# Kernel optimization log

Measured on AMD Instinct MI355X. Metric: run time of the kernel, lower is better.

The kernel has to match this reference:

```python
import math
import jax, jax.numpy as jnp
import numpy as np

FS = 96000.0
N_BIQUADS = 16
HPF_FREQ_RANGE = (20.0, 500.0)
LPF_FREQ_RANGE = (5000.0, 20000.0)
SHELF_FREQ_RANGE = (50.0, 16000.0)
PEAK_FREQ_RANGE = (100.0, 15000.0)
Q_RANGE = (0.5, 16.0)
GAIN_RANGE = (-24.0, 24.0)
BROADBAND_RANGE = (-60.0, 0.0)


def _denorm_log(norm, lo, hi):
    return jnp.exp(math.log(lo) + norm * (math.log(hi) - math.log(lo)))


def _coef_highpass(fc, Q):
    w0 = 2.0 * math.pi * fc / FS
    alpha = jnp.sin(w0) / (2.0 * Q)
    c = jnp.cos(w0)
    b0 = (1 + c) / 2; b1 = -(1 + c); b2 = (1 + c) / 2
    a0 = 1 + alpha; a1 = -2 * c; a2 = 1 - alpha
    return b0 / a0, b1 / a0, b2 / a0, a1 / a0, a2 / a0


def _coef_lowpass(fc, Q):
    w0 = 2.0 * math.pi * fc / FS
    alpha = jnp.sin(w0) / (2.0 * Q)
    c = jnp.cos(w0)
    b0 = (1 - c) / 2; b1 = 1 - c; b2 = (1 - c) / 2
    a0 = 1 + alpha; a1 = -2 * c; a2 = 1 - alpha
    return b0 / a0, b1 / a0, b2 / a0, a1 / a0, a2 / a0


def _coef_lowshelf(fc, gain_db, Q):
    A = 10.0 ** (gain_db / 40.0)
    w0 = 2.0 * math.pi * fc / FS
    alpha = jnp.sin(w0) / (2.0 * Q)
    c = jnp.cos(w0)
    sA = jnp.sqrt(A)
    b0 = A * (A + 1 - (A - 1) * c + 2 * sA * alpha)
    b1 = 2 * A * (A - 1 - (A + 1) * c)
    b2 = A * (A + 1 - (A - 1) * c - 2 * sA * alpha)
    a0 = A + 1 + (A - 1) * c + 2 * sA * alpha
    a1 = -2 * (A - 1 + (A + 1) * c)
    a2 = A + 1 + (A - 1) * c - 2 * sA * alpha
    return b0 / a0, b1 / a0, b2 / a0, a1 / a0, a2 / a0


def _coef_highshelf(fc, gain_db, Q):
    A = 10.0 ** (gain_db / 40.0)
    w0 = 2.0 * math.pi * fc / FS
    alpha = jnp.sin(w0) / (2.0 * Q)
    c = jnp.cos(w0)
    sA = jnp.sqrt(A)
    b0 = A * (A + 1 + (A - 1) * c + 2 * sA * alpha)
    b1 = -2 * A * (A - 1 + (A + 1) * c)
    b2 = A * (A + 1 + (A - 1) * c - 2 * sA * alpha)
    a0 = A + 1 - (A - 1) * c + 2 * sA * alpha
    a1 = 2 * (A - 1 - (A + 1) * c)
    a2 = A + 1 - (A - 1) * c - 2 * sA * alpha
    return b0 / a0, b1 / a0, b2 / a0, a1 / a0, a2 / a0


def _coef_peak(fc, gain_db, Q):
    A = 10.0 ** (gain_db / 40.0)
    w0 = 2.0 * math.pi * fc / FS
    alpha = jnp.sin(w0) / (2.0 * Q)
    c = jnp.cos(w0)
    b0 = 1 + alpha * A; b1 = -2 * c; b2 = 1 - alpha * A
    a0 = 1 + alpha / A; a1 = -2 * c; a2 = 1 - alpha / A
    return b0 / a0, b1 / a0, b2 / a0, a1 / a0, a2 / a0


def _biquad(x, coefs):
    # x: (B, T); coefs: 5 arrays of shape (B,)
    b0, b1, b2, a1, a2 = coefs

    def step(carry, xt):  # xt: (B,)
        s1, s2 = carry
        y = b0 * xt + s1
        return (b1 * xt - a1 * y + s2, b2 * xt - a2 * y), y

    z = jnp.zeros(x.shape[0], x.dtype)
    _, ys = jax.lax.scan(step, (z, z), x.T)  # ys: (T, B)
    return ys.T


def _chain(audio, params):
    B = audio.shape[0]
    bp = params[:, :N_BIQUADS * 3].reshape(B, N_BIQUADS, 3)
    bb_lo, bb_hi = BROADBAND_RANGE
    in_db = bb_lo + params[:, -2] * (bb_hi - bb_lo)
    out_db = bb_lo + params[:, -1] * (bb_hi - bb_lo)
    x = audio * (10.0 ** (in_db / 20.0))[:, None]

    for i in range(N_BIQUADS):
        fn, gn, qn = bp[:, i, 0], bp[:, i, 1], bp[:, i, 2]
        Q = _denorm_log(qn, *Q_RANGE)
        gain = GAIN_RANGE[0] + gn * (GAIN_RANGE[1] - GAIN_RANGE[0])
        if i == 0:  # HPF
            coefs = _coef_highpass(_denorm_log(fn, *HPF_FREQ_RANGE), Q)
        elif i == 15:  # LPF
            coefs = _coef_lowpass(_denorm_log(fn, *LPF_FREQ_RANGE), Q)
        elif i == 1:  # low shelf
            coefs = _coef_lowshelf(_denorm_log(fn, *SHELF_FREQ_RANGE), gain, Q)
        elif i == 14:  # high shelf
            coefs = _coef_highshelf(_denorm_log(fn, *SHELF_FREQ_RANGE), gain, Q)
        else:  # peaking EQ
            coefs = _coef_peak(_denorm_log(fn, *PEAK_FREQ_RANGE), gain, Q)
        x = _biquad(x, coefs)

    return x * (10.0 ** (out_db / 20.0))[:, None]


def setup_inputs() -> dict:
    key = jax.random.key(0)
    k1, k2 = jax.random.split(key)
    audio = jax.random.normal(k1, (16, 262144), dtype=jnp.float32)
    params = jax.random.uniform(k2, (16, 50), dtype=jnp.float32)
    return {"audio": audio, "params": params}


def reference(audio, params):
    return _chain(audio, params)
```

## Files before the change

### kernel.cpp

```cpp
#include <hip/hip_runtime.h>
#include <math.h>

#define BATCH   16
#define T_LEN   262144
#define NB      16
#define L       64
#define GRP     64
#define SUB     8
#define NSUB    512
#define NSUP    32
#define NG      64
#define NCHUNK  4096
#define XSTRIDE 68

#define DPI 3.14159265358979323846264338327950288

#define OFF_COEF  0
#define OFF_A64   1536
#define OFF_A512  17920
#define OFF_A8K   34304
#define OFF_QEND  50688
#define OFF_SARR  312832
#define OFF_P     574976

__device__ inline void stage_coefs(int i, double fn, double gn, double qn,
                                   double& B0, double& B1, double& B2,
                                   double& A1, double& A2) {
    const double FS = 96000.0;
    double Q    = exp(log(0.5) + qn * (log(16.0) - log(0.5)));
    double gain = -24.0 + gn * 48.0;
    double lo, hi;
    if (i == 0)            { lo = 20.0;   hi = 500.0;   }
    else if (i == 15)      { lo = 5000.0; hi = 20000.0; }
    else if (i == 1 || i == 14) { lo = 50.0; hi = 16000.0; }
    else                   { lo = 100.0;  hi = 15000.0; }
    double fc    = exp(log(lo) + fn * (log(hi) - log(lo)));
    double w0    = 2.0 * DPI * fc / FS;
    double alpha = sin(w0) / (2.0 * Q);
    double c     = cos(w0);
    double b0, b1, b2, a0, a1, a2;
    if (i == 0) {
        b0 = (1.0 + c) * 0.5; b1 = -(1.0 + c); b2 = (1.0 + c) * 0.5;
        a0 = 1.0 + alpha; a1 = -2.0 * c; a2 = 1.0 - alpha;
    } else if (i == 15) {
        b0 = (1.0 - c) * 0.5; b1 = 1.0 - c; b2 = (1.0 - c) * 0.5;
        a0 = 1.0 + alpha; a1 = -2.0 * c; a2 = 1.0 - alpha;
    } else if (i == 1) {
        double A = pow(10.0, gain / 40.0), sA = sqrt(A);
        b0 = A * ((A + 1.0) - (A - 1.0) * c + 2.0 * sA * alpha);
        b1 = 2.0 * A * ((A - 1.0) - (A + 1.0) * c);
        b2 = A * ((A + 1.0) - (A - 1.0) * c - 2.0 * sA * alpha);
        a0 = (A + 1.0) + (A - 1.0) * c + 2.0 * sA * alpha;
        a1 = -2.0 * ((A - 1.0) + (A + 1.0) * c);
        a2 = (A + 1.0) + (A - 1.0) * c - 2.0 * sA * alpha;
    } else if (i == 14) {
        double A = pow(10.0, gain / 40.0), sA = sqrt(A);
        b0 = A * ((A + 1.0) + (A - 1.0) * c + 2.0 * sA * alpha);
        b1 = -2.0 * A * ((A - 1.0) + (A + 1.0) * c);
        b2 = A * ((A + 1.0) + (A - 1.0) * c - 2.0 * sA * alpha);
        a0 = (A + 1.0) - (A - 1.0) * c + 2.0 * sA * alpha;
        a1 = 2.0 * ((A - 1.0) - (A + 1.0) * c);
        a2 = (A + 1.0) - (A - 1.0) * c - 2.0 * sA * alpha;
    } else {
        double A = pow(10.0, gain / 40.0);
        b0 = 1.0 + alpha * A; b1 = -2.0 * c; b2 = 1.0 - alpha * A;
        a0 = 1.0 + alpha / A; a1 = -2.0 * c; a2 = 1.0 - alpha / A;
    }
    B0 = b0 / a0; B1 = b1 / a0; B2 = b2 / a0; A1 = a1 / a0; A2 = a2 / a0;
}

__global__ __launch_bounds__(512) void k0_setup(const float* __restrict__ params,
                                                float* __restrict__ coefs,
                                                float* __restrict__ A64,
                                                float* __restrict__ A512,
                                                float* __restrict__ A8K) {
    int b = blockIdx.x;
    int t = threadIdx.x;
    __shared__ double cf[NB][5];
    __shared__ double M1[32 * 32];
    __shared__ double M2[32 * 32];

    if (t < NB) {
        double B0, B1, B2, A1, A2;
        stage_coefs(t, (double)params[b * 50 + t * 3 + 0],
                       (double)params[b * 50 + t * 3 + 1],
                       (double)params[b * 50 + t * 3 + 2], B0, B1, B2, A1, A2);
        float f0 = (float)B0, f1 = (float)B1, f2 = (float)B2, f3 = (float)A1, f4 = (float)A2;
        cf[t][0] = (double)f0; cf[t][1] = (double)f1; cf[t][2] = (double)f2;
        cf[t][3] = (double)f3; cf[t][4] = (double)f4;
        float* cp = coefs + b * 96 + t * 5;
        cp[0] = f0; cp[1] = f1; cp[2] = f2; cp[3] = f3; cp[4] = f4;
    }
    if (t == NB) {
        double indb = -60.0 + (double)params[b * 50 + 48] * 60.0;
        coefs[b * 96 + 80] = (float)pow(10.0, indb / 20.0);
    }
    if (t == NB + 1) {
        double outdb = -60.0 + (double)params[b * 50 + 49] * 60.0;
        coefs[b * 96 + 81] = (float)pow(10.0, outdb / 20.0);
    }
    __syncthreads();

    if (t < 32) {
        double s1[NB], s2[NB];
#pragma unroll
        for (int i = 0; i < NB; i++) {
            s1[i] = (t == 2 * i) ? 1.0 : 0.0;
            s2[i] = (t == 2 * i + 1) ? 1.0 : 0.0;
        }
        double u = 0.0;
#pragma unroll
        for (int i = 0; i < NB; i++) {
            double y  = cf[i][0] * u + s1[i];
            double n1 = cf[i][1] * u - cf[i][3] * y + s2[i];
            double n2 = cf[i][2] * u - cf[i][4] * y;
            s1[i] = n1; s2[i] = n2; u = y;
        }
#pragma unroll
        for (int i = 0; i < NB; i++) {
            M1[(2 * i) * 32 + t]     = s1[i];
            M1[(2 * i + 1) * 32 + t] = s2[i];
        }
    }
    __syncthreads();

    int c  = t & 31;
    int r0 = t >> 5;
    double* src = M1;
    double* dst = M2;
    for (int sq = 0; sq < 13; sq++) {
        double acc0 = 0.0, acc1 = 0.0;
        for (int k = 0; k < 32; k++) {
            double bv = src[k * 32 + c];
            acc0 += src[r0 * 32 + k] * bv;
            acc1 += src[(r0 + 16) * 32 + k] * bv;
        }
        dst[r0 * 32 + c]        = acc0;
        dst[(r0 + 16) * 32 + c] = acc1;
        __syncthreads();
        { double* tmp = src; src = dst; dst = tmp; }
        float* out_m = (sq == 5) ? A64 : (sq == 8) ? A512 : (sq == 12) ? A8K : nullptr;
        if (out_m) {
            int i0 = r0 * 32 + c, i1 = (r0 + 16) * 32 + c;
            out_m[b * 1024 + i0] = (float)src[i0];
            out_m[b * 1024 + i1] = (float)src[i1];
        }
        __syncthreads();
    }
}

__device__ __forceinline__ void bc_step4(float* qldsw, int row, int cb,
                                         const float* ar,
                                         float p0, float p1, float p2, float p3,
                                         float& q0, float& q1, float& q2, float& q3) {
    qldsw[(cb + 0) * 32 + row] = q0;
    qldsw[(cb + 1) * 32 + row] = q1;
    qldsw[(cb + 2) * 32 + row] = q2;
    qldsw[(cb + 3) * 32 + row] = q3;
    const float* qb = qldsw + cb * 32;
    float a0 = p0, b0 = 0.f, a1 = p1, b1 = 0.f;
    float a2 = p2, b2 = 0.f, a3 = p3, b3 = 0.f;
#pragma unroll
    for (int t4 = 0; t4 < 8; t4++) {
        float4 v0 = *(const float4*)(qb + 0 * 32 + 4 * t4);
        float4 v1 = *(const float4*)(qb + 1 * 32 + 4 * t4);
        float4 v2 = *(const float4*)(qb + 2 * 32 + 4 * t4);
        float4 v3 = *(const float4*)(qb + 3 * 32 + 4 * t4);
        a0 = fmaf(ar[4 * t4 + 0], v0.x, a0); b0 = fmaf(ar[4 * t4 + 1], v0.y, b0);
        a0 = fmaf(ar[4 * t4 + 2], v0.z, a0); b0 = fmaf(ar[4 * t4 + 3], v0.w, b0);
        a1 = fmaf(ar[4 * t4 + 0], v1.x, a1); b1 = fmaf(ar[4 * t4 + 1], v1.y, b1);
        a1 = fmaf(ar[4 * t4 + 2], v1.z, a1); b1 = fmaf(ar[4 * t4 + 3], v1.w, b1);
        a2 = fmaf(ar[4 * t4 + 0], v2.x, a2); b2 = fmaf(ar[4 * t4 + 1], v2.y, b2);
        a2 = fmaf(ar[4 * t4 + 2], v2.z, a2); b2 = fmaf(ar[4 * t4 + 3], v2.w, b2);
        a3 = fmaf(ar[4 * t4 + 0], v3.x, a3); b3 = fmaf(ar[4 * t4 + 1], v3.y, b3);
        a3 = fmaf(ar[4 * t4 + 2], v3.z, a3); b3 = fmaf(ar[4 * t4 + 3], v3.w, b3);
    }
    q0 = a0 + b0; q1 = a1 + b1; q2 = a2 + b2; q3 = a3 + b3;
}

__device__ __forceinline__ float mv_step_rl(const float* ar, float q, float addv) {
    int qi = __float_as_int(q);
    float qb[32];
#pragma unroll
    for (int t = 0; t < 32; t++)
        qb[t] = __int_as_float(__builtin_amdgcn_readlane(qi, t));
    float acc0 = addv, acc1 = 0.f;
#pragma unroll
    for (int t = 0; t < 32; t += 2) {
        acc0 = fmaf(ar[t], qb[t], acc0);
        acc1 = fmaf(ar[t + 1], qb[t + 1], acc1);
    }
    return acc0 + acc1;
}

__device__ __forceinline__ void load_row32(const float* base, int row, float* ar) {
    const float4* a4 = (const float4*)(base + row * 32);
#pragma unroll
    for (int j = 0; j < 8; j++) {
        float4 v = a4[j];
        ar[4 * j + 0] = v.x; ar[4 * j + 1] = v.y;
        ar[4 * j + 2] = v.z; ar[4 * j + 3] = v.w;
    }
}

__device__ __forceinline__ void stage_audio(const float* __restrict__ gbase,
                                            float* __restrict__ xlds, int lane) {
    const float4* g4 = (const float4*)gbase;
    float4 v[16];
#pragma unroll
    for (int it = 0; it < 16; it++) v[it] = g4[it * 64 + lane];
#pragma unroll
    for (int it = 0; it < 16; it++) {
        int idx = it * 64 + lane;
        int ch = idx >> 4, q = idx & 15;
        *(float4*)&xlds[ch * XSTRIDE + q * 4] = v[it];
    }
}

__global__ __launch_bounds__(64, 1) void k1_pass1(const float* __restrict__ audio,
                                                  const float* __restrict__ coefs,
                                                  const float* __restrict__ A64,
                                                  float* __restrict__ P,
                                                  float* __restrict__ Qend) {
    int blk   = blockIdx.x;
    int batch = blk >> 6;
    int grp   = blk & 63;
    int lane  = threadIdx.x;
    int row   = lane & 31;
    int half  = lane >> 5;

    __shared__ float xlds[GRP * XSTRIDE];
    __shared__ float plds[GRP][33];
    __shared__ float qlds[8 * 32];

    stage_audio(audio + (size_t)batch * T_LEN + (size_t)grp * GRP * L, xlds, lane);
    __syncthreads();

    const float* cf = coefs + batch * 96;
    float c0[NB], c1[NB], c2[NB], c3[NB], c4[NB];
#pragma unroll
    for (int i = 0; i < NB; i++) {
        c0[i] = cf[i * 5 + 0]; c1[i] = cf[i * 5 + 1]; c2[i] = cf[i * 5 + 2];
        c3[i] = cf[i * 5 + 3]; c4[i] = cf[i * 5 + 4];
    }
    float ing = cf[80];

    float s1[NB], s2[NB];
#pragma unroll
    for (int i = 0; i < NB; i++) { s1[i] = 0.f; s2[i] = 0.f; }

    float* xrow = &xlds[lane * XSTRIDE];
#pragma unroll 1
    for (int tt = 0; tt < 16; tt++) {
        float4 xv = *(const float4*)&xrow[tt * 4];
        float xs[4] = {xv.x, xv.y, xv.z, xv.w};
#pragma unroll
        for (int j = 0; j < 4; j++) {
            float u = ing * xs[j];
#pragma unroll
            for (int i = 0; i < NB; i++) {
                float y  = fmaf(c0[i], u, s1[i]);
                float n1 = fmaf(c1[i], u, s2[i]); n1 = fmaf(-c3[i], y, n1);
                float n2 = c2[i] * u;             n2 = fmaf(-c4[i], y, n2);
                s1[i] = n1; s2[i] = n2; u = y;
            }
        }
    }

    {
        float* pb = P + ((size_t)(batch * NG + grp)) * 2048;
#pragma unroll
        for (int i = 0; i < NB; i++) {
            pb[(2 * i) * 64 + lane]     = s1[i];
            pb[(2 * i + 1) * 64 + lane] = s2[i];
        }
    }

#pragma unroll
    for (int i = 0; i < NB; i++) {
        plds[lane][2 * i]     = s1[i];
        plds[lane][2 * i + 1] = s2[i];
    }
    __syncthreads();

    float ar[32];
    load_row32(A64 + batch * 1024, row, ar);
    int cb = half * 4;
    float q0 = plds[(cb + 0) * SUB][row];
    float q1 = plds[(cb + 1) * SUB][row];
    float q2 = plds[(cb + 2) * SUB][row];
    float q3 = plds[(cb + 3) * SUB][row];
#pragma unroll 1
    for (int j = 1; j < SUB; j++) {
        float p0 = plds[(cb + 0) * SUB + j][row];
        float p1 = plds[(cb + 1) * SUB + j][row];
        float p2 = plds[(cb + 2) * SUB + j][row];
        float p3 = plds[(cb + 3) * SUB + j][row];
        bc_step4(qlds, row, cb, ar, p0, p1, p2, p3, q0, q1, q2, q3);
    }
    {
        float* qe = Qend + ((size_t)(batch * NSUB + grp * 8 + cb)) * 32 + row;
        qe[0] = q0; qe[32] = q1; qe[64] = q2; qe[96] = q3;
    }
}

__global__ __launch_bounds__(256, 1) void k2_combine(const float* __restrict__ A512,
                                                     const float* __restrict__ A8K,
                                                     const float* __restrict__ Qend,
                                                     float* __restrict__ Sarr) {
    int batch = blockIdx.x;
    int tid   = threadIdx.x;
    int wave  = tid >> 6;
    int lane  = tid & 63;
    int row   = lane & 31;
    int half  = lane >> 5;
    int cb    = half * 4;

    __shared__ float qe[NSUB][32];
    __shared__ float qs[NSUP][32];
    __shared__ float ss[NSUP][32];
    __shared__ float qlds[4][8 * 32];

    {
        const float4* src4 = (const float4*)(Qend + (size_t)batch * NSUB * 32);
        float4* dst4 = (float4*)&qe[0][0];
        for (int i = tid; i < NSUB * 32 / 4; i += 256) dst4[i] = src4[i];
    }
    float ar512[32];
    load_row32(A512 + batch * 1024, row, ar512);
    __syncthreads();

    int sbase = wave * 8 + cb;

    {
        float q0 = qe[(sbase + 0) * 16][row];
        float q1 = qe[(sbase + 1) * 16][row];
        float q2 = qe[(sbase + 2) * 16][row];
        float q3 = qe[(sbase + 3) * 16][row];
#pragma unroll 1
        for (int j = 1; j < 16; j++) {
            float p0 = qe[(sbase + 0) * 16 + j][row];
            float p1 = qe[(sbase + 1) * 16 + j][row];
            float p2 = qe[(sbase + 2) * 16 + j][row];
            float p3 = qe[(sbase + 3) * 16 + j][row];
            bc_step4(qlds[wave], row, cb, ar512, p0, p1, p2, p3, q0, q1, q2, q3);
        }
        qs[sbase + 0][row] = q0; qs[sbase + 1][row] = q1;
        qs[sbase + 2][row] = q2; qs[sbase + 3][row] = q3;
    }
    __syncthreads();

    if (wave == 0) {
        float ark[32];
        load_row32(A8K + batch * 1024, row, ark);
        float S = 0.f;
#pragma unroll 1
        for (int s = 0; s < NSUP; s++) {
            if (lane < 32) ss[s][row] = S;
            float addv = qs[s][row];
            S = mv_step_rl(ark, S, addv);
        }
    }
    __syncthreads();

    {
        float q0 = ss[sbase + 0][row];
        float q1 = ss[sbase + 1][row];
        float q2 = ss[sbase + 2][row];
        float q3 = ss[sbase + 3][row];
#pragma unroll 1
        for (int j = 0; j < 16; j++) {
            Sarr[((size_t)(batch * NSUB + (sbase + 0) * 16 + j)) * 32 + row] = q0;
            Sarr[((size_t)(batch * NSUB + (sbase + 1) * 16 + j)) * 32 + row] = q1;
            Sarr[((size_t)(batch * NSUB + (sbase + 2) * 16 + j)) * 32 + row] = q2;
            Sarr[((size_t)(batch * NSUB + (sbase + 3) * 16 + j)) * 32 + row] = q3;
            if (j < 15) {
                float p0 = qe[(sbase + 0) * 16 + j][row];
                float p1 = qe[(sbase + 1) * 16 + j][row];
                float p2 = qe[(sbase + 2) * 16 + j][row];
                float p3 = qe[(sbase + 3) * 16 + j][row];
                bc_step4(qlds[wave], row, cb, ar512, p0, p1, p2, p3, q0, q1, q2, q3);
            }
        }
    }
}

__global__ __launch_bounds__(64, 1) void k3_pass2(const float* __restrict__ audio,
                                                  const float* __restrict__ coefs,
                                                  const float* __restrict__ A64,
                                                  const float* __restrict__ P,
                                                  const float* __restrict__ Sarr,
                                                  float* __restrict__ out) {
    int blk   = blockIdx.x;
    int batch = blk >> 6;
    int grp   = blk & 63;
    int lane  = threadIdx.x;
    int row   = lane & 31;
    int half  = lane >> 5;
    int cb    = half * 4;

    __shared__ float xlds[GRP * XSTRIDE];
    __shared__ float plds[GRP][33];
    __shared__ float qlds[8 * 32];

    stage_audio(audio + (size_t)batch * T_LEN + (size_t)grp * GRP * L, xlds, lane);

    {
        const float* pb = P + ((size_t)(batch * NG + grp)) * 2048;
        float pv[32];
#pragma unroll
        for (int s = 0; s < 32; s++) pv[s] = pb[s * 64 + lane];
#pragma unroll
        for (int s = 0; s < 32; s++) plds[lane][s] = pv[s];
    }
    __syncthreads();

    {
        float ar[32];
        load_row32(A64 + batch * 1024, row, ar);
        const float* sp = Sarr + ((size_t)(batch * NSUB + grp * 8 + cb)) * 32 + row;
        float q0 = sp[0], q1 = sp[32], q2 = sp[64], q3 = sp[96];
#pragma unroll 1
        for (int j = 0; j < SUB; j++) {
            float p0 = plds[(cb + 0) * SUB + j][row];
            float p1 = plds[(cb + 1) * SUB + j][row];
            float p2 = plds[(cb + 2) * SUB + j][row];
            float p3 = plds[(cb + 3) * SUB + j][row];
            plds[(cb + 0) * SUB + j][row] = q0;
            plds[(cb + 1) * SUB + j][row] = q1;
            plds[(cb + 2) * SUB + j][row] = q2;
            plds[(cb + 3) * SUB + j][row] = q3;
            if (j < SUB - 1)
                bc_step4(qlds, row, cb, ar, p0, p1, p2, p3, q0, q1, q2, q3);
        }
    }
    __syncthreads();

    const float* cf = coefs + batch * 96;
    float c0[NB], c1[NB], c2[NB], c3[NB], c4[NB];
#pragma unroll
    for (int i = 0; i < NB; i++) {
        c0[i] = cf[i * 5 + 0]; c1[i] = cf[i * 5 + 1]; c2[i] = cf[i * 5 + 2];
        c3[i] = cf[i * 5 + 3]; c4[i] = cf[i * 5 + 4];
    }
    float ing  = cf[80];
    float outg = cf[81];

    float s1[NB], s2[NB];
#pragma unroll
    for (int i = 0; i < NB; i++) {
        s1[i] = plds[lane][2 * i];
        s2[i] = plds[lane][2 * i + 1];
    }

    float* xrow = &xlds[lane * XSTRIDE];
#pragma unroll 1
    for (int tt = 0; tt < 16; tt++) {
        float4 xv = *(const float4*)&xrow[tt * 4];
        float xs[4] = {xv.x, xv.y, xv.z, xv.w};
        float ys[4];
#pragma unroll
        for (int j = 0; j < 4; j++) {
            float u = ing * xs[j];
#pragma unroll
            for (int i = 0; i < NB; i++) {
                float y  = fmaf(c0[i], u, s1[i]);
                float n1 = fmaf(c1[i], u, s2[i]); n1 = fmaf(-c3[i], y, n1);
                float n2 = c2[i] * u;             n2 = fmaf(-c4[i], y, n2);
                s1[i] = n1; s2[i] = n2; u = y;
            }
            ys[j] = outg * u;
        }
        float4 yv; yv.x = ys[0]; yv.y = ys[1]; yv.z = ys[2]; yv.w = ys[3];
        *(float4*)&xrow[tt * 4] = yv;
    }
    __syncthreads();

    {
        float4* g4 = (float4*)(out + (size_t)batch * T_LEN + (size_t)grp * GRP * L);
#pragma unroll
        for (int it = 0; it < 16; it++) {
            int idx = it * 64 + lane;
            int ch = idx >> 4, q = idx & 15;
            g4[it * 64 + lane] = *(const float4*)&xlds[ch * XSTRIDE + q * 4];
        }
    }
}

extern "C" void kernel_launch(void* const* d_in, const int* in_sizes, int n_in,
                              void* d_out, int out_size, void* d_ws, size_t ws_size,
                              hipStream_t stream) {
    const float* audio  = (const float*)d_in[0];
    const float* params = (const float*)d_in[1];
    float* out = (float*)d_out;
    float* ws  = (float*)d_ws;

    float* coefs = ws + OFF_COEF;
    float* A64   = ws + OFF_A64;
    float* A512  = ws + OFF_A512;
    float* A8K   = ws + OFF_A8K;
    float* Qend  = ws + OFF_QEND;
    float* Sarr  = ws + OFF_SARR;
    float* P     = ws + OFF_P;

    k0_setup<<<BATCH, 512, 0, stream>>>(params, coefs, A64, A512, A8K);
    k1_pass1<<<BATCH * NG, 64, 0, stream>>>(audio, coefs, A64, P, Qend);
    k2_combine<<<BATCH, 256, 0, stream>>>(A512, A8K, Qend, Sarr);
    k3_pass2<<<BATCH * NG, 64, 0, stream>>>(audio, coefs, A64, P, Sarr, out);
}
```

Measured before the change: 156.8 us.

## Replace second-pass IIR recompute with zero-state output plus state impulse-response correction

Measured after the change: 169.0 us. +7.8%, slower.

```diff
diff --git a/kernel.cpp b/kernel.cpp
--- a/kernel.cpp
+++ b/kernel.cpp
@@ -22,6 +22,8 @@
 #define OFF_QEND  50688
 #define OFF_SARR  312832
 #define OFF_P     574976
+#define OFF_YZ    2672128
+#define OFF_W     6866432
 
 __device__ inline void stage_coefs(int i, double fn, double gn, double qn,
                                    double& B0, double& B1, double& B2,
@@ -73,7 +75,8 @@
                                                 float* __restrict__ coefs,
                                                 float* __restrict__ A64,
                                                 float* __restrict__ A512,
-                                                float* __restrict__ A8K) {
+                                                float* __restrict__ A8K,
+                                                float* __restrict__ Wws) {
     int b = blockIdx.x;
     int t = threadIdx.x;
     __shared__ double cf[NB][5];
@@ -120,6 +123,34 @@
         for (int i = 0; i < NB; i++) {
             M1[(2 * i) * 32 + t]     = s1[i];
             M1[(2 * i + 1) * 32 + t] = s2[i];
+        }
+    } else if (t >= 64 && t < 96) {
+        int j = t - 64;
+        float fc0[NB], fc1[NB], fc2[NB], fc3[NB], fc4[NB];
+#pragma unroll
+        for (int i = 0; i < NB; i++) {
+            fc0[i] = (float)cf[i][0]; fc1[i] = (float)cf[i][1];
+            fc2[i] = (float)cf[i][2]; fc3[i] = (float)cf[i][3];
+            fc4[i] = (float)cf[i][4];
+        }
+        float s1[NB], s2[NB];
+#pragma unroll
+        for (int i = 0; i < NB; i++) {
+            s1[i] = (j == 2 * i) ? 1.f : 0.f;
+            s2[i] = (j == 2 * i + 1) ? 1.f : 0.f;
+        }
+        float* wp = Wws + (size_t)b * 2048 + j * 64;
+#pragma unroll 1
+        for (int k = 0; k < 64; k++) {
+            float u = 0.f;
+#pragma unroll
+            for (int i = 0; i < NB; i++) {
+                float y  = fmaf(fc0[i], u, s1[i]);
+                float n1 = fmaf(fc1[i], u, s2[i]); n1 = fmaf(-fc3[i], y, n1);
+                float n2 = fc2[i] * u;             n2 = fmaf(-fc4[i], y, n2);
+                s1[i] = n1; s2[i] = n2; u = y;
+            }
+            wp[k] = u;
         }
     }
     __syncthreads();
@@ -221,7 +252,8 @@
                                                   const float* __restrict__ coefs,
                                                   const float* __restrict__ A64,
                                                   float* __restrict__ P,
-                                                  float* __restrict__ Qend) {
+                                                  float* __restrict__ Qend,
+                                                  float* __restrict__ Yz) {
     int blk   = blockIdx.x;
     int batch = blk >> 6;
     int grp   = blk & 63;
@@ -254,6 +286,7 @@
     for (int tt = 0; tt < 16; tt++) {
         float4 xv = *(const float4*)&xrow[tt * 4];
         float xs[4] = {xv.x, xv.y, xv.z, xv.w};
+        float ys[4];
 #pragma unroll
         for (int j = 0; j < 4; j++) {
             float u = ing * xs[j];
@@ -264,7 +297,10 @@
                 float n2 = c2[i] * u;             n2 = fmaf(-c4[i], y, n2);
                 s1[i] = n1; s2[i] = n2; u = y;
             }
-        }
+            ys[j] = u;
+        }
+        float4 yv; yv.x = ys[0]; yv.y = ys[1]; yv.z = ys[2]; yv.w = ys[3];
+        *(float4*)&xrow[tt * 4] = yv;
     }
 
     {
@@ -282,6 +318,16 @@
         plds[lane][2 * i + 1] = s2[i];
     }
     __syncthreads();
+
+    {
+        float4* g4 = (float4*)(Yz + (size_t)batch * T_LEN + (size_t)grp * GRP * L);
+#pragma unroll
+        for (int it = 0; it < 16; it++) {
+            int idx = it * 64 + lane;
+            int ch = idx >> 4, q = idx & 15;
+            g4[idx] = *(const float4*)&xlds[ch * XSTRIDE + q * 4];
+        }
+    }
 
     float ar[32];
     load_row32(A64 + batch * 1024, row, ar);
@@ -385,9 +431,10 @@
     }
 }
 
-__global__ __launch_bounds__(64, 1) void k3_pass2(const float* __restrict__ audio,
+__global__ __launch_bounds__(64, 1) void k3_pass2(const float* __restrict__ Yz,
                                                   const float* __restrict__ coefs,
                                                   const float* __restrict__ A64,
+                                                  const float* __restrict__ Wws,
                                                   const float* __restrict__ P,
                                                   const float* __restrict__ Sarr,
                                                   float* __restrict__ out) {
@@ -402,8 +449,16 @@
     __shared__ float xlds[GRP * XSTRIDE];
     __shared__ float plds[GRP][33];
     __shared__ float qlds[8 * 32];
-
-    stage_audio(audio + (size_t)batch * T_LEN + (size_t)grp * GRP * L, xlds, lane);
+    __shared__ __align__(16) float wlds[2048];
+
+    stage_audio(Yz + (size_t)batch * T_LEN + (size_t)grp * GRP * L, xlds, lane);
+
+    {
+        const float* wsrc = Wws + (size_t)batch * 2048;
+#pragma unroll
+        for (int it = 0; it < 32; it++)
+            wlds[it * 64 + lane] = wsrc[it * 64 + lane];
+    }
 
     {
         const float* pb = P + ((size_t)(batch * NG + grp)) * 2048;
@@ -436,43 +491,41 @@
     }
     __syncthreads();
 
-    const float* cf = coefs + batch * 96;
-    float c0[NB], c1[NB], c2[NB], c3[NB], c4[NB];
-#pragma unroll
-    for (int i = 0; i < NB; i++) {
-        c0[i] = cf[i * 5 + 0]; c1[i] = cf[i * 5 + 1]; c2[i] = cf[i * 5 + 2];
-        c3[i] = cf[i * 5 + 3]; c4[i] = cf[i * 5 + 4];
-    }
-    float ing  = cf[80];
-    float outg = cf[81];
-
-    float s1[NB], s2[NB];
-#pragma unroll
-    for (int i = 0; i < NB; i++) {
-        s1[i] = plds[lane][2 * i];
-        s2[i] = plds[lane][2 * i + 1];
-    }
+    float outg = coefs[batch * 96 + 81];
+
+    float sst[32];
+#pragma unroll
+    for (int s = 0; s < 32; s++) sst[s] = plds[lane][s];
 
     float* xrow = &xlds[lane * XSTRIDE];
-#pragma unroll 1
+    float y[64];
+#pragma unroll
     for (int tt = 0; tt < 16; tt++) {
-        float4 xv = *(const float4*)&xrow[tt * 4];
-        float xs[4] = {xv.x, xv.y, xv.z, xv.w};
-        float ys[4];
-#pragma unroll
-        for (int j = 0; j < 4; j++) {
-            float u = ing * xs[j];
-#pragma unroll
-            for (int i = 0; i < NB; i++) {
-                float y  = fmaf(c0[i], u, s1[i]);
-                float n1 = fmaf(c1[i], u, s2[i]); n1 = fmaf(-c3[i], y, n1);
-                float n2 = c2[i] * u;             n2 = fmaf(-c4[i], y, n2);
-                s1[i] = n1; s2[i] = n2; u = y;
-            }
-            ys[j] = outg * u;
-        }
-        float4 yv; yv.x = ys[0]; yv.y = ys[1]; yv.z = ys[2]; yv.w = ys[3];
-        *(float4*)&xrow[tt * 4] = yv;
+        float4 v = *(const float4*)&xrow[tt * 4];
+        y[4 * tt + 0] = v.x; y[4 * tt + 1] = v.y;
+        y[4 * tt + 2] = v.z; y[4 * tt + 3] = v.w;
+    }
+
+#pragma unroll 1
+    for (int j = 0; j < 32; j++) {
+        float sj = sst[j];
+        const float* wr = &wlds[j * 64];
+#pragma unroll
+        for (int t4 = 0; t4 < 16; t4++) {
+            float4 w = *(const float4*)&wr[4 * t4];
+            y[4 * t4 + 0] = fmaf(w.x, sj, y[4 * t4 + 0]);
+            y[4 * t4 + 1] = fmaf(w.y, sj, y[4 * t4 + 1]);
+            y[4 * t4 + 2] = fmaf(w.z, sj, y[4 * t4 + 2]);
+            y[4 * t4 + 3] = fmaf(w.w, sj, y[4 * t4 + 3]);
+        }
+    }
+
+#pragma unroll
+    for (int tt = 0; tt < 16; tt++) {
+        float4 v;
+        v.x = outg * y[4 * tt + 0]; v.y = outg * y[4 * tt + 1];
+        v.z = outg * y[4 * tt + 2]; v.w = outg * y[4 * tt + 3];
+        *(float4*)&xrow[tt * 4] = v;
     }
     __syncthreads();
 
@@ -482,7 +535,7 @@
         for (int it = 0; it < 16; it++) {
             int idx = it * 64 + lane;
             int ch = idx >> 4, q = idx & 15;
-            g4[it * 64 + lane] = *(const float4*)&xlds[ch * XSTRIDE + q * 4];
+            g4[idx] = *(const float4*)&xlds[ch * XSTRIDE + q * 4];
         }
     }
 }
@@ -502,9 +555,11 @@
     float* Qend  = ws + OFF_QEND;
     float* Sarr  = ws + OFF_SARR;
     float* P     = ws + OFF_P;
-
-    k0_setup<<<BATCH, 512, 0, stream>>>(params, coefs, A64, A512, A8K);
-    k1_pass1<<<BATCH * NG, 64, 0, stream>>>(audio, coefs, A64, P, Qend);
+    float* Yz    = ws + OFF_YZ;
+    float* Wws   = ws + OFF_W;
+
+    k0_setup<<<BATCH, 512, 0, stream>>>(params, coefs, A64, A512, A8K, Wws);
+    k1_pass1<<<BATCH * NG, 64, 0, stream>>>(audio, coefs, A64, P, Qend, Yz);
     k2_combine<<<BATCH, 256, 0, stream>>>(A512, A8K, Qend, Sarr);
-    k3_pass2<<<BATCH * NG, 64, 0, stream>>>(audio, coefs, A64, P, Sarr, out);
-}
+    k3_pass2<<<BATCH * NG, 64, 0, stream>>>(Yz, coefs, A64, Wws, P, Sarr, out);
+}
```
